# Optimization experiments

Measured on AMD Instinct MI355X. Metric: run time of the kernel, lower is better.

The kernel has to match this reference:

```python
import jax, jax.numpy as jnp
import numpy as np

H = 16       # num_attention_heads
HKV = 4      # num_key_value_heads
G = H // HKV # num_kv_groups
D = 128      # head_dim
ROT = 64     # rotary dim = head_dim * rope_partial_rotary_factor (0.5)
BLK = 64     # sparse_block_size
LOCAL = 8    # sparse_local_num_blocks
GLOB = 1     # sparse_global_num_blocks
SCALE = 1.0 / float(np.sqrt(D))
NEG = -1000000000.0


def _rotate_half(x):
    x1, x2 = x[..., : x.shape[-1] // 2], x[..., x.shape[-1] // 2 :]
    return jnp.concatenate((-x2, x1), axis=-1)


def _sparse_tables(n_blocks):
    """Static numpy tables mirroring _get_sparse_tables + causal masking.
    Returns idx (n,S) int32 gather table and mask (n, BLK, S, BLK) bool (True = masked)."""
    S = LOCAL + GLOB
    idx = np.zeros((n_blocks, S), np.int32)
    valid = np.zeros((n_blocks, S), bool)
    for i in range(n_blocks):
        sel = [g for g in range(GLOB) if g < n_blocks]
        sel += list(range(max(0, i - (LOCAL - 1)), i + 1))
        li = list(dict.fromkeys(sel))  # dedupe, keep order
        idx[i, : len(li)] = li
        valid[i, : len(li)] = True
    ii = np.arange(n_blocks)[:, None]
    dead = (~valid) | (idx > ii)          # invalid slot or future block
    selfb = idx == ii                     # diagonal block -> intra-causal
    jq = np.arange(BLK)[:, None]
    jk = np.arange(BLK)[None, :]
    intra = jk > jq                       # (q, k) strictly-upper masked
    mask = dead[:, None, :, None] | (selfb[:, None, :, None] & intra[None, :, None, :])
    return idx, mask                      # (n,S), (n,BLK,S,BLK)


def setup_inputs() -> dict:
    key = jax.random.key(0)
    ks = jax.random.split(key, 6)
    B_, T, HID = 2, 4096, 2048
    hidden_states = jax.random.normal(ks[0], (B_, T, HID), dtype=jnp.float32)
    # real RoPE tables for the rotary sub-dim
    inv_freq = 1.0 / (10000.0 ** (np.arange(0, ROT, 2, dtype=np.float32) / ROT))
    freqs = np.arange(T, dtype=np.float32)[:, None] * inv_freq[None, :]
    emb = np.concatenate([freqs, freqs], axis=-1)  # (T, ROT)
    cos = jnp.broadcast_to(jnp.asarray(np.cos(emb)), (B_, T, ROT))
    sin = jnp.broadcast_to(jnp.asarray(np.sin(emb)), (B_, T, ROT))
    Wq = jax.random.normal(ks[1], (H * D, HID), dtype=jnp.float32) * 0.02
    Wk = jax.random.normal(ks[2], (HKV * D, HID), dtype=jnp.float32) * 0.02
    Wv = jax.random.normal(ks[3], (HKV * D, HID), dtype=jnp.float32) * 0.02
    Wo = jax.random.normal(ks[4], (HID, H * D), dtype=jnp.float32) * 0.02
    return {"hidden_states": hidden_states, "cos": cos, "sin": sin,
            "Wq": Wq, "Wk": Wk, "Wv": Wv, "Wo": Wo}


def reference(hidden_states, cos, sin, Wq, Wk, Wv, Wo):
    B_, T, _ = hidden_states.shape
    q = (hidden_states @ Wq.T).reshape(B_, T, H, D).transpose(0, 2, 1, 3)    # (b,H,T,D)
    k = (hidden_states @ Wk.T).reshape(B_, T, HKV, D).transpose(0, 2, 1, 3)  # (b,HKV,T,D)
    v = (hidden_states @ Wv.T).reshape(B_, T, HKV, D).transpose(0, 2, 1, 3)
    # partial RoPE on first ROT dims
    c = cos[:, None, :, :]
    s = sin[:, None, :, :]
    def rope(x):
        xr, xp = x[..., :ROT], x[..., ROT:]
        xr = xr * c + _rotate_half(xr) * s
        return jnp.concatenate([xr, xp], axis=-1)
    q, k = rope(q), rope(k)
    # block-sparse local+global attention (prefill, T multiple of BLK)
    n = T // BLK
    idx_np, mask_np = _sparse_tables(n)
    idx = jnp.asarray(idx_np)
    mask = jnp.asarray(mask_np)  # (n, BLKq, S, BLKk)
    qb = q.reshape(B_, HKV, G, n, BLK, D)
    kb = k.reshape(B_, HKV, n, BLK, D)
    vb = v.reshape(B_, HKV, n, BLK, D)
    ksel = kb[:, :, idx]  # (b,HKV,n,S,BLK,D)
    vsel = vb[:, :, idx]
    scores = jnp.einsum('bhgnqd,bhnskd->bhgnqsk',
                        qb.astype(jnp.float32), ksel.astype(jnp.float32)) * SCALE
    scores = jnp.where(mask[None, None, None], NEG, scores)
    sh = scores.shape
    probs = jax.nn.softmax(scores.reshape(*sh[:5], -1), axis=-1).reshape(sh)
    out = jnp.einsum('bhgnqsk,bhnskd->bhgnqd', probs, vsel.astype(jnp.float32))
    out = out.astype(hidden_states.dtype).reshape(B_, H, T, D)
    out = out.transpose(0, 2, 1, 3).reshape(B_, T, H * D)
    return out @ Wo.T
```

## Files before the change

### kernel.cpp

```cpp
#include <hip/hip_runtime.h>
#include <hip/hip_bf16.h>

#define Hq   16
#define HKV  4
#define Dh   128
#define ROT  64
#define BLKQ 64
#define NBLK 64
#define Tlen 4096
#define Bsz  2
#define HID  2048
#define QKVC 3072
#define SCALE_C 0.08838834764831845f

typedef __attribute__((ext_vector_type(8))) short bf16x8;
typedef __attribute__((ext_vector_type(4))) float f32x4;

#define MFMA16(a, b, c) __builtin_amdgcn_mfma_f32_16x16x32_bf16((a), (b), (c), 0, 0, 0)

__device__ __forceinline__ void async_copy16(__hip_bfloat16* lds, const __hip_bfloat16* g) {
    __builtin_amdgcn_global_load_lds(
        (const __attribute__((address_space(1))) void*)g,
        (__attribute__((address_space(3))) void*)lds,
        16, 0, 0);
}

__global__ __launch_bounds__(256) void cvt_kernel(
    const float* __restrict__ s0, const float* __restrict__ s1,
    const float* __restrict__ s2, const float* __restrict__ s3,
    const float* __restrict__ s4,
    __hip_bfloat16* __restrict__ base,
    int n0, int n1, int n2, int n3, int n4)
{
    const float* src;
    size_t off, n;
    switch (blockIdx.y) {
        case 0:  src = s0; off = 0;                          n = n0; break;
        case 1:  src = s1; off = (size_t)n0;                 n = n1; break;
        case 2:  src = s2; off = (size_t)n0 + n1;            n = n2; break;
        case 3:  src = s3; off = (size_t)n0 + n1 + n2;       n = n3; break;
        default: src = s4; off = (size_t)n0 + n1 + n2 + n3;  n = n4; break;
    }
    __hip_bfloat16* dst = base + off;
    const size_t stride = (size_t)gridDim.x * 2048;
    for (size_t i = ((size_t)blockIdx.x * 256 + threadIdx.x) * 8; i < n; i += stride) {
        const float4 a = *(const float4*)(src + i);
        const float4 b = *(const float4*)(src + i + 4);
        union { bf16x8 v; __hip_bfloat16 e[8]; } u;
        u.e[0] = __float2bfloat16(a.x); u.e[1] = __float2bfloat16(a.y);
        u.e[2] = __float2bfloat16(a.z); u.e[3] = __float2bfloat16(a.w);
        u.e[4] = __float2bfloat16(b.x); u.e[5] = __float2bfloat16(b.y);
        u.e[6] = __float2bfloat16(b.z); u.e[7] = __float2bfloat16(b.w);
        *(bf16x8*)(dst + i) = u.v;
    }
}

template <bool ROPE, bool F32OUT>
__global__ __launch_bounds__(256) void gemm_bt(
    const __hip_bfloat16* __restrict__ A,
    const __hip_bfloat16* __restrict__ B0,
    const __hip_bfloat16* __restrict__ B1,
    const __hip_bfloat16* __restrict__ B2,
    int n1c, int n2c,
    void* __restrict__ C,
    int M, int N, int K,
    const float* __restrict__ cosb,
    const float* __restrict__ sinb)
{
    __shared__ __align__(16) __hip_bfloat16 As[128 * 64];
    __shared__ __align__(16) __hip_bfloat16 Bs[128 * 64];

    const int m0 = blockIdx.y * 128;
    const int n0 = blockIdx.x * 128;
    const __hip_bfloat16* Bp;
    int nb;
    if (n0 < n1c)      { Bp = B0; nb = n0; }
    else if (n0 < n2c) { Bp = B1; nb = n0 - n1c; }
    else               { Bp = B2; nb = n0 - n2c; }

    const int tid  = threadIdx.x;
    const int lane = tid & 63;
    const int w    = tid >> 6;
    const int wm   = (w >> 1) * 64;
    const int wn   = (w & 1) * 64;
    const int lr   = lane >> 3;
    const int lc   = lane & 7;
    const int m16  = lane & 15;
    const int q8   = lane >> 4;

    f32x4 acc[4][4] = {};

    for (int k0 = 0; k0 < K; k0 += 64) {
        __syncthreads();
        for (int ii = 0; ii < 4; ++ii) {
            const int r8 = w * 32 + ii * 8;
            const int r  = r8 + lr;
            const int cg = lc ^ (r & 7);
            async_copy16(&As[r8 * 64], A  + (size_t)(m0 + r) * K + k0 + cg * 8);
            async_copy16(&Bs[r8 * 64], Bp + (size_t)(nb + r) * K + k0 + cg * 8);
        }
        __syncthreads();

        for (int ks = 0; ks < 2; ++ks) {
            bf16x8 af[4], bfr[4];
            for (int t = 0; t < 4; ++t) {
                const int row = wm + t * 16 + m16;
                const int csA = (ks * 4 + q8) ^ (row & 7);
                af[t] = *(const bf16x8*)&As[row * 64 + csA * 8];
                const int col = wn + t * 16 + m16;
                const int csB = (ks * 4 + q8) ^ (col & 7);
                bfr[t] = *(const bf16x8*)&Bs[col * 64 + csB * 8];
            }
            for (int i = 0; i < 4; ++i)
                for (int j = 0; j < 4; ++j)
                    acc[i][j] = MFMA16(af[i], bfr[j], acc[i][j]);
        }
    }

    if (ROPE && n0 < n2c && wn == 0) {
        for (int i = 0; i < 4; ++i)
            for (int r = 0; r < 4; ++r) {
                const int bt = m0 + wm + i * 16 + q8 * 4 + r;
                for (int j = 0; j < 2; ++j) {
                    const int d = j * 16 + m16;
                    const float c = cosb[(size_t)bt * ROT + d];
                    const float s = sinb[(size_t)bt * ROT + d];
                    const float x1 = acc[i][j][r];
                    const float x2 = acc[i][j + 2][r];
                    acc[i][j][r]     = x1 * c - x2 * s;
                    acc[i][j + 2][r] = x2 * c + x1 * s;
                }
            }
    }

    for (int i = 0; i < 4; ++i)
        for (int j = 0; j < 4; ++j)
            for (int r = 0; r < 4; ++r) {
                const int row = m0 + wm + i * 16 + q8 * 4 + r;
                const int col = n0 + wn + j * 16 + m16;
                if (F32OUT)
                    ((float*)C)[(size_t)row * N + col] = acc[i][j][r];
                else
                    ((__hip_bfloat16*)C)[(size_t)row * N + col] =
                        __float2bfloat16(acc[i][j][r]);
            }
}

__global__ __launch_bounds__(256) void attn_kernel(
    const __hip_bfloat16* __restrict__ qkv,
    __hip_bfloat16* __restrict__ outb)
{
    const int i   = blockIdx.x;
    const int h   = blockIdx.y;
    const int b   = blockIdx.z;
    const int kvh = h >> 2;
    const int tid  = threadIdx.x;
    const int lane = tid & 63;
    const int w    = tid >> 6;
    const int m16  = lane & 15;
    const int q8   = lane >> 4;

    __shared__ __align__(16) __hip_bfloat16 Ks[64 * 136];
    __shared__ __align__(16) __hip_bfloat16 VT[128 * 72];
    __shared__ __align__(16) __hip_bfloat16 Pb[4][16 * 72];

    bf16x8 qf[4];
    {
        const __hip_bfloat16* qp =
            qkv + (size_t)(b * Tlen + i * BLKQ + w * 16 + m16) * QKVC + h * Dh + q8 * 8;
        for (int ks = 0; ks < 4; ++ks) qf[ks] = *(const bf16x8*)(qp + ks * 32);
    }

    f32x4 o[8] = {};
    float mrow[4] = {-1e30f, -1e30f, -1e30f, -1e30f};
    float lrow[4] = {0.f, 0.f, 0.f, 0.f};

    const int nsel = (i + 1 < 9) ? (i + 1) : 9;
    for (int j = 0; j < nsel; ++j) {
        const int kb = (i <= 7) ? j : ((j == 0) ? 0 : (i - 8 + j));

        __syncthreads();
        {
            const __hip_bfloat16* kbase =
                qkv + (size_t)(b * Tlen + kb * BLKQ) * QKVC + HID + kvh * Dh;
            const __hip_bfloat16* vbase = kbase + 512;
            for (int c = tid; c < 1024; c += 256) {
                const int key = c >> 4;
                const int d0  = (c & 15) * 8;
                *(bf16x8*)&Ks[key * 136 + d0] =
                    *(const bf16x8*)(kbase + (size_t)key * QKVC + d0);
            }
            for (int c = tid; c < 1024; c += 256) {
                const int key = c & 63;
                const int d0  = (c >> 6) * 8;
                bf16x8 v8 = *(const bf16x8*)(vbase + (size_t)key * QKVC + d0);
                const __hip_bfloat16* ve = (const __hip_bfloat16*)&v8;
                for (int jj = 0; jj < 8; ++jj)
                    VT[(d0 + jj) * 72 + key] = ve[jj];
            }
        }
        __syncthreads();

        float sv[4][4];
        for (int nt = 0; nt < 4; ++nt) {
            f32x4 s = {0.f, 0.f, 0.f, 0.f};
            for (int ks = 0; ks < 4; ++ks) {
                bf16x8 kf = *(const bf16x8*)&Ks[(nt * 16 + m16) * 136 + ks * 32 + q8 * 8];
                s = MFMA16(qf[ks], kf, s);
            }
            for (int r = 0; r < 4; ++r) sv[nt][r] = s[r] * SCALE_C;
        }
        if (kb == i) {
            for (int nt = 0; nt < 4; ++nt) {
                const int key = nt * 16 + m16;
                for (int r = 0; r < 4; ++r) {
                    const int qr = w * 16 + q8 * 4 + r;
                    if (key > qr) sv[nt][r] = -1e9f;
                }
            }
        }

        float alpha[4];
        for (int r = 0; r < 4; ++r) {
            float mx = fmaxf(fmaxf(sv[0][r], sv[1][r]), fmaxf(sv[2][r], sv[3][r]));
            for (int off = 1; off < 16; off <<= 1) mx = fmaxf(mx, __shfl_xor(mx, off, 64));
            const float newm = fmaxf(mrow[r], mx);
            alpha[r] = __expf(mrow[r] - newm);
            mrow[r] = newm;
            float rs = 0.f;
            for (int nt = 0; nt < 4; ++nt) {
                const float p = __expf(sv[nt][r] - newm);
                sv[nt][r] = p;
                rs += p;
            }
            for (int off = 1; off < 16; off <<= 1) rs += __shfl_xor(rs, off, 64);
            lrow[r] = lrow[r] * alpha[r] + rs;
        }

        __hip_bfloat16* Pw = &Pb[w][0];
        for (int nt = 0; nt < 4; ++nt)
            for (int r = 0; r < 4; ++r)
                Pw[(q8 * 4 + r) * 72 + nt * 16 + m16] = __float2bfloat16(sv[nt][r]);

        for (int dt = 0; dt < 8; ++dt)
            for (int r = 0; r < 4; ++r)
                o[dt][r] *= alpha[r];

        __syncthreads();

        for (int kk = 0; kk < 2; ++kk) {
            bf16x8 pf = *(const bf16x8*)&Pw[m16 * 72 + kk * 32 + q8 * 8];
            for (int dt = 0; dt < 8; ++dt) {
                bf16x8 vf = *(const bf16x8*)&VT[(dt * 16 + m16) * 72 + kk * 32 + q8 * 8];
                o[dt] = MFMA16(pf, vf, o[dt]);
            }
        }
    }

    float rcp[4];
    for (int r = 0; r < 4; ++r) rcp[r] = 1.0f / lrow[r];
    __hip_bfloat16* op = outb + (size_t)(b * Tlen + i * BLKQ) * (Hq * Dh) + h * Dh;
    for (int dt = 0; dt < 8; ++dt)
        for (int r = 0; r < 4; ++r) {
            const float val = o[dt][r] * rcp[r];
            op[(size_t)(w * 16 + q8 * 4 + r) * (Hq * Dh) + dt * 16 + m16] =
                __float2bfloat16(val);
        }
}

extern "C" void kernel_launch(void* const* d_in, const int* in_sizes, int n_in,
                              void* d_out, int out_size, void* d_ws, size_t ws_size,
                              hipStream_t stream) {
    const float* hs   = (const float*)d_in[0];
    const float* cosb = (const float*)d_in[1];
    const float* sinb = (const float*)d_in[2];
    const float* Wq   = (const float*)d_in[3];
    const float* Wk   = (const float*)d_in[4];
    const float* Wv   = (const float*)d_in[5];
    const float* Wo   = (const float*)d_in[6];

    const int M = Bsz * Tlen;
    const int nHS = M * HID;
    const int nWq = Hq * Dh * HID;
    const int nWk = HKV * Dh * HID;
    const int nWv = nWk;
    const int nWo = HID * Hq * Dh;

    __hip_bfloat16* hsb  = (__hip_bfloat16*)d_ws;
    __hip_bfloat16* wqb  = hsb + nHS;
    __hip_bfloat16* wkb  = wqb + nWq;
    __hip_bfloat16* wvb  = wkb + nWk;
    __hip_bfloat16* wob  = wvb + nWv;
    __hip_bfloat16* qkv  = wob + nWo;
    __hip_bfloat16* attn = qkv + (size_t)M * QKVC;

    cvt_kernel<<<dim3(8192, 5), 256, 0, stream>>>(
        hs, Wq, Wk, Wv, Wo, hsb, nHS, nWq, nWk, nWv, nWo);
    gemm_bt<true, false><<<dim3(QKVC / 128, M / 128), 256, 0, stream>>>(
        hsb, wqb, wkb, wvb, HID, HID + 512, qkv, M, QKVC, HID, cosb, sinb);
    attn_kernel<<<dim3(NBLK, Hq, Bsz), 256, 0, stream>>>(qkv, attn);
    gemm_bt<false, true><<<dim3(HID / 128, M / 128), 256, 0, stream>>>(
        attn, wob, wob, wob, HID, HID, d_out, M, HID, HID, nullptr, nullptr);
}
```

Measured before the change: 492.8 us.

## Replace GEMM with 256x256 tile, double-buffered, interleaved MFMA/load schedule

Replaces the 128x128 single-buffered GEMM with a 512-thread 256x256 tile kernel. It double-buffers LDS, interleaves async global-to-LDS loads with MFMA phases under explicit barriers and priority hints, and adds a block-index swizzle for L2 locality. The goal is to hide load latency and raise data reuse per tile for both projection GEMMs. In exchange it uses more LDS and registers, so occupancy drops, and the larger tiles leave fewer workgroups to spread across CUs.

```diff
diff --git a/kernel.cpp b/kernel.cpp
--- a/kernel.cpp
+++ b/kernel.cpp
@@ -55,8 +55,8 @@
     }
 }
 
-template <bool ROPE, bool F32OUT>
-__global__ __launch_bounds__(256) void gemm_bt(
+template <bool ROPE_, bool F32OUT>
+__global__ __launch_bounds__(512) void gemm256(
     const __hip_bfloat16* __restrict__ A,
     const __hip_bfloat16* __restrict__ B0,
     const __hip_bfloat16* __restrict__ B1,
@@ -67,11 +67,18 @@
     const float* __restrict__ cosb,
     const float* __restrict__ sinb)
 {
-    __shared__ __align__(16) __hip_bfloat16 As[128 * 64];
-    __shared__ __align__(16) __hip_bfloat16 Bs[128 * 64];
-
-    const int m0 = blockIdx.y * 128;
-    const int n0 = blockIdx.x * 128;
+    __shared__ __align__(16) __hip_bfloat16 As[2][256 * 64];
+    __shared__ __align__(16) __hip_bfloat16 Bs[2][256 * 64];
+
+    const int gn  = N >> 8;
+    const int nwg = (M >> 8) * gn;
+    const int id  = blockIdx.x;
+    const int swz = (id & 7) * (nwg >> 3) + (id >> 3);
+    const int mt  = swz / gn;
+    const int nt  = swz - mt * gn;
+    const int m0  = mt << 8;
+    const int n0  = nt << 8;
+
     const __hip_bfloat16* Bp;
     int nb;
     if (n0 < n1c)      { Bp = B0; nb = n0; }
@@ -81,48 +88,134 @@
     const int tid  = threadIdx.x;
     const int lane = tid & 63;
     const int w    = tid >> 6;
-    const int wm   = (w >> 1) * 64;
-    const int wn   = (w & 1) * 64;
+    const int wm   = (w >> 2) << 7;
+    const int wn   = (w & 3) << 6;
+    const int m16  = lane & 15;
+    const int q8   = lane >> 4;
     const int lr   = lane >> 3;
     const int lc   = lane & 7;
-    const int m16  = lane & 15;
-    const int q8   = lane >> 4;
-
-    f32x4 acc[4][4] = {};
-
-    for (int k0 = 0; k0 < K; k0 += 64) {
-        __syncthreads();
-        for (int ii = 0; ii < 4; ++ii) {
-            const int r8 = w * 32 + ii * 8;
-            const int r  = r8 + lr;
-            const int cg = lc ^ (r & 7);
-            async_copy16(&As[r8 * 64], A  + (size_t)(m0 + r) * K + k0 + cg * 8);
-            async_copy16(&Bs[r8 * 64], Bp + (size_t)(nb + r) * K + k0 + cg * 8);
-        }
-        __syncthreads();
-
-        for (int ks = 0; ks < 2; ++ks) {
-            bf16x8 af[4], bfr[4];
-            for (int t = 0; t < 4; ++t) {
-                const int row = wm + t * 16 + m16;
-                const int csA = (ks * 4 + q8) ^ (row & 7);
-                af[t] = *(const bf16x8*)&As[row * 64 + csA * 8];
-                const int col = wn + t * 16 + m16;
-                const int csB = (ks * 4 + q8) ^ (col & 7);
-                bfr[t] = *(const bf16x8*)&Bs[col * 64 + csB * 8];
-            }
-            for (int i = 0; i < 4; ++i)
-                for (int j = 0; j < 4; ++j)
-                    acc[i][j] = MFMA16(af[i], bfr[j], acc[i][j]);
-        }
-    }
-
-    if (ROPE && n0 < n2c && wn == 0) {
-        for (int i = 0; i < 4; ++i)
+    const int cg   = lc ^ lr;
+    const int NT   = K >> 6;
+
+    f32x4 acc[8][4] = {};
+
+    auto stageA = [&](int buf, int half, int kc) {
+        #pragma unroll
+        for (int is = 0; is < 2; ++is) {
+            const int r8 = (half << 7) + (is << 6) + (w << 3);
+            async_copy16(&As[buf][r8 << 6],
+                         A + (size_t)(m0 + r8 + lr) * K + kc + (cg << 3));
+        }
+    };
+    auto stageB = [&](int buf, int half, int kc) {
+        #pragma unroll
+        for (int is = 0; is < 2; ++is) {
+            const int r8 = (half << 7) + (is << 6) + (w << 3);
+            async_copy16(&Bs[buf][r8 << 6],
+                         Bp + (size_t)(nb + r8 + lr) * K + kc + (cg << 3));
+        }
+    };
+
+    stageA(0, 0, 0);  stageA(0, 1, 0);
+    stageB(0, 0, 0);  stageB(0, 1, 0);
+    stageA(1, 0, 64); stageA(1, 1, 64);
+    asm volatile("s_waitcnt vmcnt(4)" ::: "memory");
+    __builtin_amdgcn_s_barrier();
+
+    for (int u = 0; u < NT; ++u) {
+        const int P = u & 1;
+        int tB = u + 1; if (tB >= NT) tB -= NT;
+        int tA = u + 2; if (tA >= NT) tA -= NT;
+        const int kB = tB << 6;
+        const int kA = tA << 6;
+        const __hip_bfloat16* Ap_ = As[P];
+        const __hip_bfloat16* Bq_ = Bs[P];
+        const int csl = m16 & 7;
+
+        bf16x8 a0[8], b0[4], a1[8], b1[4];
+
+        #pragma unroll
+        for (int m = 0; m < 8; ++m) {
+            const int row = wm + (m << 4) + m16;
+            const int cs  = q8 ^ csl;
+            a0[m] = *(const bf16x8*)&Ap_[(row << 6) + (cs << 3)];
+        }
+        #pragma unroll
+        for (int n = 0; n < 4; ++n) {
+            const int row = wn + (n << 4) + m16;
+            const int cs  = q8 ^ csl;
+            b0[n] = *(const bf16x8*)&Bq_[(row << 6) + (cs << 3)];
+        }
+        stageB(P ^ 1, 0, kB);
+        __builtin_amdgcn_s_barrier();
+        asm volatile("s_waitcnt lgkmcnt(0)" ::: "memory");
+        __builtin_amdgcn_s_setprio(1);
+        #pragma unroll
+        for (int m = 0; m < 8; ++m) {
+            acc[m][0] = MFMA16(a0[m], b0[0], acc[m][0]);
+            acc[m][1] = MFMA16(a0[m], b0[1], acc[m][1]);
+        }
+        __builtin_amdgcn_s_setprio(0);
+        __builtin_amdgcn_s_barrier();
+
+        #pragma unroll
+        for (int m = 0; m < 8; ++m) {
+            const int row = wm + (m << 4) + m16;
+            const int cs  = (4 + q8) ^ csl;
+            a1[m] = *(const bf16x8*)&Ap_[(row << 6) + (cs << 3)];
+        }
+        stageB(P ^ 1, 1, kB);
+        __builtin_amdgcn_s_barrier();
+        __builtin_amdgcn_s_setprio(1);
+        #pragma unroll
+        for (int m = 0; m < 8; ++m) {
+            acc[m][2] = MFMA16(a0[m], b0[2], acc[m][2]);
+            acc[m][3] = MFMA16(a0[m], b0[3], acc[m][3]);
+        }
+        __builtin_amdgcn_s_setprio(0);
+        __builtin_amdgcn_s_barrier();
+
+        #pragma unroll
+        for (int n = 0; n < 4; ++n) {
+            const int row = wn + (n << 4) + m16;
+            const int cs  = (4 + q8) ^ csl;
+            b1[n] = *(const bf16x8*)&Bq_[(row << 6) + (cs << 3)];
+        }
+        __builtin_amdgcn_s_barrier();
+        asm volatile("s_waitcnt lgkmcnt(0)" ::: "memory");
+        __builtin_amdgcn_s_setprio(1);
+        #pragma unroll
+        for (int m = 0; m < 8; ++m) {
+            acc[m][0] = MFMA16(a1[m], b1[0], acc[m][0]);
+            acc[m][1] = MFMA16(a1[m], b1[1], acc[m][1]);
+        }
+        __builtin_amdgcn_s_setprio(0);
+        __builtin_amdgcn_s_barrier();
+
+        stageA(P, 0, kA);
+        stageA(P, 1, kA);
+        asm volatile("s_waitcnt vmcnt(4)" ::: "memory");
+        __builtin_amdgcn_s_barrier();
+        __builtin_amdgcn_s_setprio(1);
+        #pragma unroll
+        for (int m = 0; m < 8; ++m) {
+            acc[m][2] = MFMA16(a1[m], b1[2], acc[m][2]);
+            acc[m][3] = MFMA16(a1[m], b1[3], acc[m][3]);
+        }
+        __builtin_amdgcn_s_setprio(0);
+        __builtin_amdgcn_s_barrier();
+    }
+
+    const int c0 = n0 + wn;
+    if (ROPE_ && c0 < n2c && (c0 & 64) == 0) {
+        #pragma unroll
+        for (int i = 0; i < 8; ++i)
+            #pragma unroll
             for (int r = 0; r < 4; ++r) {
-                const int bt = m0 + wm + i * 16 + q8 * 4 + r;
+                const int bt = m0 + wm + (i << 4) + (q8 << 2) + r;
+                #pragma unroll
                 for (int j = 0; j < 2; ++j) {
-                    const int d = j * 16 + m16;
+                    const int d = (j << 4) + m16;
                     const float c = cosb[(size_t)bt * ROT + d];
                     const float s = sinb[(size_t)bt * ROT + d];
                     const float x1 = acc[i][j][r];
@@ -133,11 +226,14 @@
             }
     }
 
-    for (int i = 0; i < 4; ++i)
+    #pragma unroll
+    for (int i = 0; i < 8; ++i)
+        #pragma unroll
         for (int j = 0; j < 4; ++j)
+            #pragma unroll
             for (int r = 0; r < 4; ++r) {
-                const int row = m0 + wm + i * 16 + q8 * 4 + r;
-                const int col = n0 + wn + j * 16 + m16;
+                const int row = m0 + wm + (i << 4) + (q8 << 2) + r;
+                const int col = n0 + wn + (j << 4) + m16;
                 if (F32OUT)
                     ((float*)C)[(size_t)row * N + col] = acc[i][j][r];
                 else
@@ -296,9 +392,9 @@
 
     cvt_kernel<<<dim3(8192, 5), 256, 0, stream>>>(
         hs, Wq, Wk, Wv, Wo, hsb, nHS, nWq, nWk, nWv, nWo);
-    gemm_bt<true, false><<<dim3(QKVC / 128, M / 128), 256, 0, stream>>>(
+    gemm256<true, false><<<dim3((QKVC / 256) * (M / 256)), 512, 0, stream>>>(
         hsb, wqb, wkb, wvb, HID, HID + 512, qkv, M, QKVC, HID, cosb, sinb);
     attn_kernel<<<dim3(NBLK, Hq, Bsz), 256, 0, stream>>>(qkv, attn);
-    gemm_bt<false, true><<<dim3(HID / 128, M / 128), 256, 0, stream>>>(
+    gemm256<false, true><<<dim3((HID / 256) * (M / 256)), 512, 0, stream>>>(
         attn, wob, wob, wob, HID, HID, d_out, M, HID, HID, nullptr, nullptr);
 }
```

After: 479.8 us. 1.03x faster.

## Double-buffer GEMM LDS tiles and prefetch K/V with pre-transposed V

Applied to the files above, without the earlier changes.

The GEMM now keeps two LDS buffers and issues async loads for the next K-tile while the current tile's MFMAs run, raising the MFMA instruction priority around the compute. A new kernel writes a transposed copy of V to workspace once, so the attention kernel reads V already transposed instead of scattering it element by element into LDS per head. The attention loop also prefetches the next K/V block into registers during compute. The cost is an extra kernel launch, an extra workspace buffer, more registers and twice the GEMM LDS.

```diff
diff --git a/kernel.cpp b/kernel.cpp
--- a/kernel.cpp
+++ b/kernel.cpp
@@ -55,8 +55,8 @@
     }
 }
 
-template <bool ROPE, bool F32OUT>
-__global__ __launch_bounds__(256) void gemm_bt(
+template <bool ROPE_, bool F32OUT>
+__global__ __launch_bounds__(256, 2) void gemm128db(
     const __hip_bfloat16* __restrict__ A,
     const __hip_bfloat16* __restrict__ B0,
     const __hip_bfloat16* __restrict__ B1,
@@ -67,8 +67,8 @@
     const float* __restrict__ cosb,
     const float* __restrict__ sinb)
 {
-    __shared__ __align__(16) __hip_bfloat16 As[128 * 64];
-    __shared__ __align__(16) __hip_bfloat16 Bs[128 * 64];
+    __shared__ __align__(16) __hip_bfloat16 As[2][128 * 64];
+    __shared__ __align__(16) __hip_bfloat16 Bs[2][128 * 64];
 
     const int m0 = blockIdx.y * 128;
     const int n0 = blockIdx.x * 128;
@@ -87,40 +87,91 @@
     const int lc   = lane & 7;
     const int m16  = lane & 15;
     const int q8   = lane >> 4;
+    const int NT   = K >> 6;
 
     f32x4 acc[4][4] = {};
 
-    for (int k0 = 0; k0 < K; k0 += 64) {
-        __syncthreads();
+    auto stageA = [&](int buf, int kc) {
+        #pragma unroll
         for (int ii = 0; ii < 4; ++ii) {
             const int r8 = w * 32 + ii * 8;
             const int r  = r8 + lr;
             const int cg = lc ^ (r & 7);
-            async_copy16(&As[r8 * 64], A  + (size_t)(m0 + r) * K + k0 + cg * 8);
-            async_copy16(&Bs[r8 * 64], Bp + (size_t)(nb + r) * K + k0 + cg * 8);
-        }
-        __syncthreads();
-
-        for (int ks = 0; ks < 2; ++ks) {
-            bf16x8 af[4], bfr[4];
-            for (int t = 0; t < 4; ++t) {
-                const int row = wm + t * 16 + m16;
-                const int csA = (ks * 4 + q8) ^ (row & 7);
-                af[t] = *(const bf16x8*)&As[row * 64 + csA * 8];
-                const int col = wn + t * 16 + m16;
-                const int csB = (ks * 4 + q8) ^ (col & 7);
-                bfr[t] = *(const bf16x8*)&Bs[col * 64 + csB * 8];
-            }
-            for (int i = 0; i < 4; ++i)
-                for (int j = 0; j < 4; ++j)
-                    acc[i][j] = MFMA16(af[i], bfr[j], acc[i][j]);
-        }
-    }
-
-    if (ROPE && n0 < n2c && wn == 0) {
+            async_copy16(&As[buf][r8 * 64], A + (size_t)(m0 + r) * K + kc + cg * 8);
+        }
+    };
+    auto stageB = [&](int buf, int kc) {
+        #pragma unroll
+        for (int ii = 0; ii < 4; ++ii) {
+            const int r8 = w * 32 + ii * 8;
+            const int r  = r8 + lr;
+            const int cg = lc ^ (r & 7);
+            async_copy16(&Bs[buf][r8 * 64], Bp + (size_t)(nb + r) * K + kc + cg * 8);
+        }
+    };
+
+    stageA(0, 0);
+    stageB(0, 0);
+    asm volatile("s_waitcnt vmcnt(0)" ::: "memory");
+    __builtin_amdgcn_s_barrier();
+
+    for (int u = 0; u < NT; ++u) {
+        const int P  = u & 1;
+        const int kN = (u + 1 < NT ? u + 1 : 0) << 6;
+        const __hip_bfloat16* Ap_ = As[P];
+        const __hip_bfloat16* Bq_ = Bs[P];
+
+        bf16x8 a0[4], b0[4], a1[4], b1[4];
+
+        #pragma unroll
+        for (int t = 0; t < 4; ++t) {
+            const int row = wm + t * 16 + m16;
+            const int csA = q8 ^ (row & 7);
+            a0[t] = *(const bf16x8*)&Ap_[row * 64 + csA * 8];
+            const int col = wn + t * 16 + m16;
+            const int csB = q8 ^ (col & 7);
+            b0[t] = *(const bf16x8*)&Bq_[col * 64 + csB * 8];
+        }
+        stageA(P ^ 1, kN);
+        asm volatile("s_waitcnt lgkmcnt(0)" ::: "memory");
+        __builtin_amdgcn_s_setprio(1);
+        #pragma unroll
         for (int i = 0; i < 4; ++i)
+            #pragma unroll
+            for (int j = 0; j < 4; ++j)
+                acc[i][j] = MFMA16(a0[i], b0[j], acc[i][j]);
+        __builtin_amdgcn_s_setprio(0);
+
+        #pragma unroll
+        for (int t = 0; t < 4; ++t) {
+            const int row = wm + t * 16 + m16;
+            const int csA = (4 + q8) ^ (row & 7);
+            a1[t] = *(const bf16x8*)&Ap_[row * 64 + csA * 8];
+            const int col = wn + t * 16 + m16;
+            const int csB = (4 + q8) ^ (col & 7);
+            b1[t] = *(const bf16x8*)&Bq_[col * 64 + csB * 8];
+        }
+        stageB(P ^ 1, kN);
+        asm volatile("s_waitcnt lgkmcnt(0)" ::: "memory");
+        __builtin_amdgcn_s_setprio(1);
+        #pragma unroll
+        for (int i = 0; i < 4; ++i)
+            #pragma unroll
+            for (int j = 0; j < 4; ++j)
+                acc[i][j] = MFMA16(a1[i], b1[j], acc[i][j]);
+        __builtin_amdgcn_s_setprio(0);
+
+        asm volatile("s_waitcnt vmcnt(0)" ::: "memory");
+        __builtin_amdgcn_s_barrier();
+    }
+
+    if (ROPE_ && n0 < n2c && wn == 0) {
+        #pragma unroll
+        for (int i = 0; i < 4; ++i)
+            #pragma unroll
             for (int r = 0; r < 4; ++r) {
                 const int bt = m0 + wm + i * 16 + q8 * 4 + r;
+                #pragma unroll
                 for (int j = 0; j < 2; ++j) {
                     const int d = j * 16 + m16;
                     const float c = cosb[(size_t)bt * ROT + d];
@@ -133,8 +184,11 @@
             }
     }
 
+    #pragma unroll
     for (int i = 0; i < 4; ++i)
+        #pragma unroll
         for (int j = 0; j < 4; ++j)
+            #pragma unroll
             for (int r = 0; r < 4; ++r) {
                 const int row = m0 + wm + i * 16 + q8 * 4 + r;
                 const int col = n0 + wn + j * 16 + m16;
@@ -146,8 +200,32 @@
             }
 }
 
-__global__ __launch_bounds__(256) void attn_kernel(
+__global__ __launch_bounds__(256) void vtrans_kernel(
     const __hip_bfloat16* __restrict__ qkv,
+    __hip_bfloat16* __restrict__ vtg)
+{
+    const int tb = blockIdx.x;
+    const int pr = blockIdx.y;
+    const __hip_bfloat16* src =
+        qkv + ((size_t)(pr >> 2) * Tlen + tb * 64) * QKVC + HID + 512 + (pr & 3) * Dh;
+    __hip_bfloat16* dst = vtg + (size_t)pr * Dh * Tlen + tb * 64;
+    const int tid = threadIdx.x;
+    #pragma unroll
+    for (int t2 = 0; t2 < 4; ++t2) {
+        const int c  = tid + t2 * 256;
+        const int d  = c >> 3;
+        const int t0 = (c & 7) * 8;
+        union { bf16x8 v; __hip_bfloat16 e[8]; } u;
+        #pragma unroll
+        for (int j = 0; j < 8; ++j)
+            u.e[j] = src[(size_t)(t0 + j) * QKVC + d];
+        *(bf16x8*)(dst + (size_t)d * Tlen + t0) = u.v;
+    }
+}
+
+__global__ __launch_bounds__(256, 3) void attn_kernel(
+    const __hip_bfloat16* __restrict__ qkv,
+    const __hip_bfloat16* __restrict__ vtg,
     __hip_bfloat16* __restrict__ outb)
 {
     const int i   = blockIdx.x;
@@ -176,32 +254,55 @@
     float lrow[4] = {0.f, 0.f, 0.f, 0.f};
 
     const int nsel = (i + 1 < 9) ? (i + 1) : 9;
+    auto kb_of = [&](int j) { return (i <= 7) ? j : ((j == 0) ? 0 : (i - 8 + j)); };
+
+    const __hip_bfloat16* vtbase = vtg + (size_t)(b * HKV + kvh) * Dh * Tlen;
+
+    bf16x8 kr[4], vr[4];
+    {
+        const int kb0 = kb_of(0);
+        const __hip_bfloat16* kbase =
+            qkv + (size_t)(b * Tlen + kb0 * BLKQ) * QKVC + HID + kvh * Dh;
+        #pragma unroll
+        for (int t = 0; t < 4; ++t) {
+            const int c = tid + t * 256;
+            kr[t] = *(const bf16x8*)(kbase + (size_t)(c >> 4) * QKVC + (c & 15) * 8);
+            vr[t] = *(const bf16x8*)(vtbase + (size_t)(c >> 3) * Tlen
+                                     + kb0 * BLKQ + (c & 7) * 8);
+        }
+    }
+
     for (int j = 0; j < nsel; ++j) {
-        const int kb = (i <= 7) ? j : ((j == 0) ? 0 : (i - 8 + j));
+        const int kb = kb_of(j);
 
         __syncthreads();
-        {
+        #pragma unroll
+        for (int t = 0; t < 4; ++t) {
+            const int c = tid + t * 256;
+            *(bf16x8*)&Ks[(c >> 4) * 136 + (c & 15) * 8] = kr[t];
+        }
+        #pragma unroll
+        for (int t = 0; t < 4; ++t) {
+            const int c = tid + t * 256;
+            *(bf16x8*)&VT[(c >> 3) * 72 + (c & 7) * 8] = vr[t];
+        }
+        __syncthreads();
+
+        if (j + 1 < nsel) {
+            const int kbn = kb_of(j + 1);
             const __hip_bfloat16* kbase =
-                qkv + (size_t)(b * Tlen + kb * BLKQ) * QKVC + HID + kvh * Dh;
-            const __hip_bfloat16* vbase = kbase + 512;
-            for (int c = tid; c < 1024; c += 256) {
-                const int key = c >> 4;
-                const int d0  = (c & 15) * 8;
-                *(bf16x8*)&Ks[key * 136 + d0] =
-                    *(const bf16x8*)(kbase + (size_t)key * QKVC + d0);
-            }
-            for (int c = tid; c < 1024; c += 256) {
-                const int key = c & 63;
-                const int d0  = (c >> 6) * 8;
-                bf16x8 v8 = *(const bf16x8*)(vbase + (size_t)key * QKVC + d0);
-                const __hip_bfloat16* ve = (const __hip_bfloat16*)&v8;
-                for (int jj = 0; jj < 8; ++jj)
-                    VT[(d0 + jj) * 72 + key] = ve[jj];
-            }
-        }
-        __syncthreads();
+                qkv + (size_t)(b * Tlen + kbn * BLKQ) * QKVC + HID + kvh * Dh;
+            #pragma unroll
+            for (int t = 0; t < 4; ++t) {
+                const int c = tid + t * 256;
+                kr[t] = *(const bf16x8*)(kbase + (size_t)(c >> 4) * QKVC + (c & 15) * 8);
+                vr[t] = *(const bf16x8*)(vtbase + (size_t)(c >> 3) * Tlen
+                                         + kbn * BLKQ + (c & 7) * 8);
+            }
+        }
 
         float sv[4][4];
+        __builtin_amdgcn_s_setprio(1);
         for (int nt = 0; nt < 4; ++nt) {
             f32x4 s = {0.f, 0.f, 0.f, 0.f};
             for (int ks = 0; ks < 4; ++ks) {
@@ -210,6 +311,7 @@
             }
             for (int r = 0; r < 4; ++r) sv[nt][r] = s[r] * SCALE_C;
         }
+        __builtin_amdgcn_s_setprio(0);
         if (kb == i) {
             for (int nt = 0; nt < 4; ++nt) {
                 const int key = nt * 16 + m16;
@@ -246,8 +348,10 @@
             for (int r = 0; r < 4; ++r)
                 o[dt][r] *= alpha[r];
 
-        __syncthreads();
-
+        asm volatile("s_waitcnt lgkmcnt(0)" ::: "memory");
+        __builtin_amdgcn_sched_barrier(0);
+
+        __builtin_amdgcn_s_setprio(1);
         for (int kk = 0; kk < 2; ++kk) {
             bf16x8 pf = *(const bf16x8*)&Pw[m16 * 72 + kk * 32 + q8 * 8];
             for (int dt = 0; dt < 8; ++dt) {
@@ -255,6 +359,7 @@
                 o[dt] = MFMA16(pf, vf, o[dt]);
             }
         }
+        __builtin_amdgcn_s_setprio(0);
     }
 
     float rcp[4];
@@ -293,12 +398,14 @@
     __hip_bfloat16* wob  = wvb + nWv;
     __hip_bfloat16* qkv  = wob + nWo;
     __hip_bfloat16* attn = qkv + (size_t)M * QKVC;
+    __hip_bfloat16* vtg  = attn + (size_t)M * (Hq * Dh);
 
     cvt_kernel<<<dim3(8192, 5), 256, 0, stream>>>(
         hs, Wq, Wk, Wv, Wo, hsb, nHS, nWq, nWk, nWv, nWo);
-    gemm_bt<true, false><<<dim3(QKVC / 128, M / 128), 256, 0, stream>>>(
+    gemm128db<true, false><<<dim3(QKVC / 128, M / 128), 256, 0, stream>>>(
         hsb, wqb, wkb, wvb, HID, HID + 512, qkv, M, QKVC, HID, cosb, sinb);
-    attn_kernel<<<dim3(NBLK, Hq, Bsz), 256, 0, stream>>>(qkv, attn);
-    gemm_bt<false, true><<<dim3(HID / 128, M / 128), 256, 0, stream>>>(
+    vtrans_kernel<<<dim3(NBLK, Bsz * HKV), 256, 0, stream>>>(qkv, vtg);
+    attn_kernel<<<dim3(NBLK, Hq, Bsz), 256, 0, stream>>>(qkv, vtg, attn);
+    gemm128db<false, true><<<dim3(HID / 128, M / 128), 256, 0, stream>>>(
         attn, wob, wob, wob, HID, HID, d_out, M, HID, HID, nullptr, nullptr);
 }
```

Measured after the change: 430.1 us. 12.7% less time.
